# Kernel optimization log

Measured on AMD Instinct MI355X. Metric: run time of the kernel, lower is better.

Reference implementation:

```python
import jax, jax.numpy as jnp
from jax import lax
import numpy as np

B, S, D, H2, V = 1024, 256, 128, 5, 50257
EPS = 1e-5


def setup_inputs() -> dict:
    key = jax.random.key(0)
    ks = jax.random.split(key, 12)
    s = 0.08  # init scale ~ 1/sqrt(D)
    return {
        "x": jax.random.randint(ks[0], (B, S), 0, V),
        "emb": jax.random.normal(ks[1], (V, D), jnp.float32) * s,
        "W_ih1": jax.random.normal(ks[2], (D, D), jnp.float32) * s,
        "b_ih1": jax.random.normal(ks[3], (D,), jnp.float32) * s,
        "W_hh1": jax.random.normal(ks[4], (D, D), jnp.float32) * s,
        "b_hh1": jax.random.normal(ks[5], (D,), jnp.float32) * s,
        "g1": jnp.ones((D,), jnp.float32),
        "be1": jnp.zeros((D,), jnp.float32),
        "W_ih2": jax.random.normal(ks[6], (H2, D), jnp.float32) * s,
        "b_ih2": jax.random.normal(ks[7], (H2,), jnp.float32) * s,
        "W_hh2": jax.random.normal(ks[8], (H2, H2), jnp.float32) * s,
        "b_hh2": jax.random.normal(ks[9], (H2,), jnp.float32) * s,
        "g2": jnp.ones((H2,), jnp.float32),
        "be2": jnp.zeros((H2,), jnp.float32),
    }


def _rnn(xproj, W_hh):
    """Vanilla tanh RNN. xproj: [B,S,H] = x @ W_ih^T + b_ih + b_hh (precomputed)."""
    h0 = jnp.zeros((xproj.shape[0], W_hh.shape[0]), xproj.dtype)

    def step(h, xt):  # xt: [B,H]
        h = jnp.tanh(xt + h @ W_hh.T)
        return h, h

    _, hs = lax.scan(step, h0, jnp.swapaxes(xproj, 0, 1))  # [S,B,H]
    return jnp.swapaxes(hs, 0, 1)  # [B,S,H]


def _ln(z, g, b):
    m = jnp.mean(z, axis=-1, keepdims=True)
    v = jnp.mean(jnp.square(z - m), axis=-1, keepdims=True)
    return (z - m) * lax.rsqrt(v + EPS) * g + b


def reference(x, emb, W_ih1, b_ih1, W_hh1, b_hh1, g1, be1,
              W_ih2, b_ih2, W_hh2, b_hh2, g2, be2):
    e = emb[x]  # [B,S,D]
    z = _rnn(e @ W_ih1.T + (b_ih1 + b_hh1), W_hh1)
    z = _ln(z, g1, be1)
    z = _rnn(z @ W_ih2.T + (b_ih2 + b_hh2), W_hh2)  # [B,S,5]
    z = _ln(z, g2, be2)
    pooled = jnp.mean(z, axis=1)  # AvgPool1d over full seq -> [B,5]
    return jax.nn.softmax(pooled, axis=1)
```

## Files before the change

kernel.cpp:

```cpp
#include <hip/hip_runtime.h>
#include <stdint.h>

#define S_LEN 256
#define DIM   128
#define EPSL  1e-5f

typedef __bf16 bf16x8 __attribute__((ext_vector_type(8)));
typedef float  f32x4  __attribute__((ext_vector_type(4)));

__device__ __forceinline__ unsigned short f2bf_bits(float f) {
  union { float f; unsigned int u; } v; v.f = f;
  unsigned int r = v.u + 0x7fffu + ((v.u >> 16) & 1u);
  return (unsigned short)(r >> 16);
}
__device__ __forceinline__ unsigned f2bf_rhu(float f) {
  return (__float_as_uint(f) + 0x8000u) >> 16;
}
__device__ __forceinline__ unsigned pack_rhu(float lo, float hi) {
  return __builtin_amdgcn_perm(__float_as_uint(hi) + 0x8000u,
                               __float_as_uint(lo) + 0x8000u, 0x07060302u);
}
__device__ __forceinline__ float tanh_fast(float x) {
  float e = __expf(2.f * x);
  return 1.f - 2.f * __builtin_amdgcn_rcpf(e + 1.f);
}

template<int CTRL>
__device__ __forceinline__ float dpp_rot_add(float v) {
  int r = __builtin_amdgcn_update_dpp(0, __float_as_int(v), CTRL, 0xF, 0xF, true);
  return v + __int_as_float(r);
}
template<int CTRL>
__device__ __forceinline__ float dpp_rot_max(float v) {
  int r = __builtin_amdgcn_update_dpp(0, __float_as_int(v), CTRL, 0xF, 0xF, true);
  return fmaxf(v, __int_as_float(r));
}
__device__ __forceinline__ float dpp_sum16(float v) {
  v = dpp_rot_add<0x124>(v); v = dpp_rot_add<0x128>(v);
  v = dpp_rot_add<0x39>(v);  v = dpp_rot_add<0x4E>(v);
  return v;
}
__device__ __forceinline__ float dpp_max16(float v) {
  v = dpp_rot_max<0x124>(v); v = dpp_rot_max<0x128>(v);
  v = dpp_rot_max<0x39>(v);  v = dpp_rot_max<0x4E>(v);
  return v;
}
template<int CTRL>
__device__ __forceinline__ void red_level7(float& s, float& sq, float* d) {
  s  = dpp_rot_add<CTRL>(s);
  sq = dpp_rot_add<CTRL>(sq);
#pragma unroll
  for (int j = 0; j < 5; j++) d[j] = dpp_rot_add<CTRL>(d[j]);
}
template<int JJ>
__device__ __forceinline__ float bcast16(float v) {
  int r = __builtin_amdgcn_ds_swizzle(__float_as_int(v), (JJ << 5) | 0x10);
  return __int_as_float(r);
}

union Frag8 { unsigned short us[8]; bf16x8 v; int4 i4; };

__global__ __launch_bounds__(512, 2)
void rnn_main(const int* __restrict__ x, const float* __restrict__ emb,
              const float* __restrict__ Wih1, const float* __restrict__ bih1,
              const float* __restrict__ Whh1, const float* __restrict__ bhh1,
              const float* __restrict__ g1, const float* __restrict__ be1,
              const float* __restrict__ Wih2, const float* __restrict__ bih2,
              const float* __restrict__ Whh2, const float* __restrict__ bhh2,
              const float* __restrict__ g2, const float* __restrict__ be2,
              unsigned short* __restrict__ hout, int* flags,
              float* __restrict__ out)
{
  __shared__ __align__(16) unsigned short h_bf[2][16 * 128];
  __shared__ __align__(16) unsigned short e_bf[2][16 * 128];
  __shared__ int x_tile[16 * 256];
  __shared__ __align__(16) float p_lds[8][2][32][8];

  const int tid  = threadIdx.x;
  const int wave = tid >> 6;
  const int lane = tid & 63;
  const int l15  = lane & 15;
  const int q    = lane >> 4;

  if (blockIdx.x < 64) {
    const int r0 = blockIdx.x * 16;
    for (int i = tid; i < 16 * 256; i += 512)
      x_tile[i] = x[(size_t)(r0 + (i >> 8)) * S_LEN + (i & 255)];
    for (int i = tid; i < 16 * 128; i += 512) h_bf[1][i] = 0;

    const int n1 = wave * 16 + l15;
    const float bias1v = bih1[n1] + bhh1[n1];
    bf16x8 wh[4], wih[4];
#pragma unroll
    for (int kt = 0; kt < 4; kt++) {
      int k0 = kt * 32 + q * 8;
      Frag8 fh, fa;
#pragma unroll
      for (int j = 0; j < 8; j++) {
        fh.us[j] = f2bf_bits(Whh1[n1 * DIM + k0 + j]);
        fa.us[j] = f2bf_bits(Wih1[n1 * DIM + k0 + j]);
      }
      wh[kt] = fh.v; wih[kt] = fa.v;
    }

    const int srow = wave * 2 + (lane >> 5);
    const int soct = (lane >> 1) & 15;
    const int ssub = lane & 1;
    const int sdst = srow * 128 + ((soct ^ srow) & 15) * 8 + ssub * 4;
    float4 pf[2];
    __syncthreads();

    {
      float4 ta, tb;
      { int xid = x_tile[srow * 256 + 0];
        ta = *(const float4*)(emb + (size_t)xid * DIM + soct * 8 + ssub * 4); }
      { int xid = x_tile[srow * 256 + 1];
        tb = *(const float4*)(emb + (size_t)xid * DIM + soct * 8 + ssub * 4); }
      { int xid = x_tile[srow * 256 + 2];
        pf[0] = *(const float4*)(emb + (size_t)xid * DIM + soct * 8 + ssub * 4); }
      { int xid = x_tile[srow * 256 + 3];
        pf[1] = *(const float4*)(emb + (size_t)xid * DIM + soct * 8 + ssub * 4); }
      int2 pa, pb;
      pa.x = (int)pack_rhu(ta.x, ta.y); pa.y = (int)pack_rhu(ta.z, ta.w);
      pb.x = (int)pack_rhu(tb.x, tb.y); pb.y = (int)pack_rhu(tb.z, tb.w);
      *(int2*)&e_bf[0][sdst] = pa;
      *(int2*)&e_bf[1][sdst] = pb;
    }
    __syncthreads();

    f32x4 xpacc = {bias1v, bias1v, bias1v, bias1v};
#pragma unroll
    for (int kt = 0; kt < 4; kt++) {
      int sw = (((kt * 4 + q) ^ l15) & 15) * 8;
      bf16x8 ae = *(const bf16x8*)&e_bf[0][l15 * 128 + sw];
      xpacc = __builtin_amdgcn_mfma_f32_16x16x32_bf16(ae, wih[kt], xpacc, 0, 0, 0);
    }
    asm volatile("s_waitcnt lgkmcnt(0)\n\ts_barrier" ::: "memory");

#pragma unroll 2
    for (int t = 0; t < S_LEN; t++) {
      f32x4 acc = xpacc;
      {
        const int rb = (t + 1) & 1;
#pragma unroll
        for (int kt = 0; kt < 4; kt++) {
          int sw = (((kt * 4 + q) ^ l15) & 15) * 8;
          bf16x8 ahf = *(const bf16x8*)&h_bf[rb][l15 * 128 + sw];
          acc = __builtin_amdgcn_mfma_f32_16x16x32_bf16(ahf, wh[kt], acc, 0, 0, 0);
        }
        const int wb = t & 1;
        const int oct = n1 >> 3;
#pragma unroll
        for (int r = 0; r < 4; r++) {
          int row = q * 4 + r;
          unsigned short us = (unsigned short)f2bf_rhu(tanh_fast(acc[r]));
          h_bf[wb][row * 128 + ((oct ^ row) & 15) * 8 + (n1 & 7)] = us;
          hout[((size_t)(r0 + row) * S_LEN + t) * DIM + n1] = us;
        }
      }

      if (t + 1 < S_LEN) {
        f32x4 a = {bias1v, bias1v, bias1v, bias1v};
#pragma unroll
        for (int kt = 0; kt < 4; kt++) {
          int sw = (((kt * 4 + q) ^ l15) & 15) * 8;
          bf16x8 ae = *(const bf16x8*)&e_bf[(t + 1) & 1][l15 * 128 + sw];
          a = __builtin_amdgcn_mfma_f32_16x16x32_bf16(ae, wih[kt], a, 0, 0, 0);
        }
        xpacc = a;
      }

      {
        if (t + 2 < S_LEN) {
          int2 pk;
          pk.x = (int)pack_rhu(pf[t & 1].x, pf[t & 1].y);
          pk.y = (int)pack_rhu(pf[t & 1].z, pf[t & 1].w);
          *(int2*)&e_bf[t & 1][sdst] = pk;
        }
        if (t + 4 < S_LEN) {
          int xid = x_tile[srow * 256 + t + 4];
          pf[t & 1] = *(const float4*)(emb + (size_t)xid * DIM + soct * 8 + ssub * 4);
        }
      }
      if (flags != nullptr && (t & 31) == 31)
        asm volatile("s_waitcnt vmcnt(0)" ::: "memory");
      asm volatile("s_waitcnt lgkmcnt(0)\n\ts_barrier" ::: "memory");
      if (flags != nullptr && (t & 31) == 31 && tid == 0)
        __hip_atomic_store(&flags[blockIdx.x * 8 + (t >> 5)], (t >> 5) + 1,
                           __ATOMIC_RELEASE, __HIP_MEMORY_SCOPE_AGENT);
    }
  } else {
    const int bt = blockIdx.x - 64;
    float w2g[5][8], Gs[5], Bs[5], wrow[5];
#pragma unroll
    for (int j = 0; j < 8; j++) {
      int c = l15 * 8 + j;
      float gc = g1[c];
#pragma unroll
      for (int jj = 0; jj < 5; jj++) w2g[jj][j] = Wih2[jj * DIM + c] * gc;
    }
#pragma unroll
    for (int jj = 0; jj < 5; jj++) { Gs[jj] = 0.f; Bs[jj] = 0.f; }
    for (int c = 0; c < DIM; c++) {
      float gc = g1[c], bc = be1[c];
#pragma unroll
      for (int jj = 0; jj < 5; jj++) {
        float w = Wih2[jj * DIM + c];
        Gs[jj] += w * gc; Bs[jj] += w * bc;
      }
    }
    const float validf = (l15 < 5) ? 1.f : 0.f;
    float t2_l = 0.f, g2_l = 0.f, be2_l = 0.f;
    if (l15 < 5) {
      t2_l = bih2[l15] + bhh2[l15];
      g2_l = g2[l15]; be2_l = be2[l15];
#pragma unroll
      for (int jj = 0; jj < 5; jj++) wrow[jj] = Whh2[l15 * 5 + jj];
    } else {
#pragma unroll
      for (int jj = 0; jj < 5; jj++) wrow[jj] = 0.f;
    }
    float h2rep[5] = {0, 0, 0, 0, 0}, pool_l = 0.f;
    const int row_l = 2 * wave + (q & 1);
    const unsigned short* hb =
        hout + (size_t)(bt * 16 + row_l) * S_LEN * DIM;
    const int idx = (l15 < 5) ? l15 : 0;

    for (int c8 = 0; c8 < 8; c8++) {
      if (tid == 0) {
        while (__hip_atomic_load(&flags[bt * 8 + c8], __ATOMIC_RELAXED,
                                 __HIP_MEMORY_SCOPE_AGENT) < c8 + 1)
          __builtin_amdgcn_s_sleep(2);
      }
      __syncthreads();
      __builtin_amdgcn_fence(__ATOMIC_ACQUIRE, "agent");
      for (int tt = 0; tt < 16; tt++) {
        int toff = tt * 2 + (q >> 1);
        uint4 cur = *(const uint4*)(hb + (size_t)(c8 * 32 + toff) * DIM + l15 * 8);
        float hv[8];
        hv[0] = __uint_as_float(cur.x << 16); hv[1] = __uint_as_float(cur.x & 0xffff0000u);
        hv[2] = __uint_as_float(cur.y << 16); hv[3] = __uint_as_float(cur.y & 0xffff0000u);
        hv[4] = __uint_as_float(cur.z << 16); hv[5] = __uint_as_float(cur.z & 0xffff0000u);
        hv[6] = __uint_as_float(cur.w << 16); hv[7] = __uint_as_float(cur.w & 0xffff0000u);
        float s = 0.f, sq = 0.f, d[5] = {0, 0, 0, 0, 0};
#pragma unroll
        for (int j = 0; j < 8; j++) {
          float v = hv[j];
          s += v; sq += v * v;
#pragma unroll
          for (int jj = 0; jj < 5; jj++) d[jj] = fmaf(w2g[jj][j], v, d[jj]);
        }
        red_level7<0x124>(s, sq, d);
        red_level7<0x128>(s, sq, d);
        red_level7<0x39>(s, sq, d);
        red_level7<0x4E>(s, sq, d);
        float mean = s * (1.f / 128.f);
        float var  = sq * (1.f / 128.f) - mean * mean;
        float rstd = rsqrtf(var + EPSL);
        float p[5];
#pragma unroll
        for (int jj = 0; jj < 5; jj++)
          p[jj] = rstd * (d[jj] - mean * Gs[jj]) + Bs[jj];
        float psel = (l15 == 0) ? p[0] : (l15 == 1) ? p[1] :
                     (l15 == 2) ? p[2] : (l15 == 3) ? p[3] : p[4];
        if (l15 < 5) p_lds[wave][q & 1][toff][l15] = psel;
      }
      asm volatile("s_waitcnt lgkmcnt(0)" ::: "memory");
      for (int s = 0; s < 32; s++) {
        float pv = p_lds[wave][q & 1][s][idx];
        float a = pv + t2_l;
#pragma unroll
        for (int jj = 0; jj < 5; jj++) a = fmaf(wrow[jj], h2rep[jj], a);
        float xn = tanh_fast(a);
        float s2 = dpp_sum16(xn * validf) * 0.2f;
        float dd = xn - s2;
        float v2 = dpp_sum16(dd * dd * validf) * 0.2f;
        float r2 = rsqrtf(v2 + EPSL);
        pool_l += dd * r2 * g2_l + be2_l;
        h2rep[0] = bcast16<0>(xn); h2rep[1] = bcast16<1>(xn);
        h2rep[2] = bcast16<2>(xn); h2rep[3] = bcast16<3>(xn);
        h2rep[4] = bcast16<4>(xn);
      }
    }
    float lg = pool_l * (1.f / 256.f);
    float mx = dpp_max16((l15 < 5) ? lg : -3.0e38f);
    float e  = (l15 < 5) ? __expf(lg - mx) : 0.f;
    float sm = dpp_sum16(e);
    if (q < 2 && l15 < 5)
      out[(size_t)(bt * 16 + row_l) * 5 + l15] = e / sm;
  }
}

__global__ __launch_bounds__(256, 2)
void rnn_tail_r11(const unsigned short* __restrict__ hall,
                  const float* __restrict__ g1,  const float* __restrict__ be1,
                  const float* __restrict__ Wih2, const float* __restrict__ bih2,
                  const float* __restrict__ Whh2, const float* __restrict__ bhh2,
                  const float* __restrict__ g2,  const float* __restrict__ be2,
                  float* __restrict__ out)
{
  __shared__ float p_lds[4][4][8];
  const int tid  = threadIdx.x;
  const int wave = tid >> 6;
  const int lane = tid & 63;
  const int l15  = lane & 15;
  const int q    = lane >> 4;
  const int b    = blockIdx.x * 4 + wave;

  float w2g[5][8], Gs[5], Bs[5], wrow[5];
#pragma unroll
  for (int j = 0; j < 8; j++) {
    int c = l15 * 8 + j;
    float gc = g1[c];
#pragma unroll
    for (int jj = 0; jj < 5; jj++) w2g[jj][j] = Wih2[jj * DIM + c] * gc;
  }
#pragma unroll
  for (int jj = 0; jj < 5; jj++) { Gs[jj] = 0.f; Bs[jj] = 0.f; }
  for (int c = 0; c < DIM; c++) {
    float gc = g1[c], bc = be1[c];
#pragma unroll
    for (int jj = 0; jj < 5; jj++) {
      float w = Wih2[jj * DIM + c];
      Gs[jj] += w * gc; Bs[jj] += w * bc;
    }
  }
  const float validf = (l15 < 5) ? 1.f : 0.f;
  float t2_l = 0.f, g2_l = 0.f, be2_l = 0.f;
  if (l15 < 5) {
    t2_l = bih2[l15] + bhh2[l15];
    g2_l = g2[l15]; be2_l = be2[l15];
#pragma unroll
    for (int jj = 0; jj < 5; jj++) wrow[jj] = Whh2[l15 * 5 + jj];
  } else {
#pragma unroll
    for (int jj = 0; jj < 5; jj++) wrow[jj] = 0.f;
  }
  float h2rep[5];
#pragma unroll
  for (int jj = 0; jj < 5; jj++) h2rep[jj] = 0.f;
  float pool_l = 0.f;

  const unsigned short* hb = hall + (size_t)b * S_LEN * DIM;
  uint4 hpre = *(const uint4*)(hb + (size_t)q * DIM + l15 * 8);

  for (int t0 = 0; t0 < S_LEN; t0 += 4) {
    uint4 cur = hpre;
    if (t0 + 4 < S_LEN)
      hpre = *(const uint4*)(hb + (size_t)(t0 + 4 + q) * DIM + l15 * 8);
    float hv[8];
    hv[0] = __uint_as_float(cur.x << 16); hv[1] = __uint_as_float(cur.x & 0xffff0000u);
    hv[2] = __uint_as_float(cur.y << 16); hv[3] = __uint_as_float(cur.y & 0xffff0000u);
    hv[4] = __uint_as_float(cur.z << 16); hv[5] = __uint_as_float(cur.z & 0xffff0000u);
    hv[6] = __uint_as_float(cur.w << 16); hv[7] = __uint_as_float(cur.w & 0xffff0000u);
    float s = 0.f, sq = 0.f, d[5] = {0, 0, 0, 0, 0};
#pragma unroll
    for (int j = 0; j < 8; j++) {
      float v = hv[j];
      s += v; sq += v * v;
#pragma unroll
      for (int jj = 0; jj < 5; jj++) d[jj] = fmaf(w2g[jj][j], v, d[jj]);
    }
    red_level7<0x124>(s, sq, d);
    red_level7<0x128>(s, sq, d);
    red_level7<0x39>(s, sq, d);
    red_level7<0x4E>(s, sq, d);
    float mean = s * (1.f / 128.f);
    float var  = sq * (1.f / 128.f) - mean * mean;
    float rstd = rsqrtf(var + EPSL);
    float p[5];
#pragma unroll
    for (int jj = 0; jj < 5; jj++)
      p[jj] = rstd * (d[jj] - mean * Gs[jj]) + Bs[jj];
    float psel = (l15 == 0) ? p[0] : (l15 == 1) ? p[1] :
                 (l15 == 2) ? p[2] : (l15 == 3) ? p[3] : p[4];
    if (l15 < 5) p_lds[wave][q][l15] = psel;
    asm volatile("s_waitcnt lgkmcnt(0)" ::: "memory");
    const int idx = (l15 < 5) ? l15 : 0;
#pragma unroll
    for (int g = 0; g < 4; g++) {
      float pv = p_lds[wave][g][idx];
      float a = pv + t2_l;
#pragma unroll
      for (int jj = 0; jj < 5; jj++) a = fmaf(wrow[jj], h2rep[jj], a);
      float xn = tanh_fast(a);
      float s2 = dpp_sum16(xn * validf) * 0.2f;
      float dd = xn - s2;
      float v2 = dpp_sum16(dd * dd * validf) * 0.2f;
      float r2 = rsqrtf(v2 + EPSL);
      pool_l += dd * r2 * g2_l + be2_l;
      h2rep[0] = bcast16<0>(xn); h2rep[1] = bcast16<1>(xn);
      h2rep[2] = bcast16<2>(xn); h2rep[3] = bcast16<3>(xn);
      h2rep[4] = bcast16<4>(xn);
    }
  }

  float lg = pool_l * (1.f / 256.f);
  float mx = dpp_max16((l15 < 5) ? lg : -3.0e38f);
  float e  = (l15 < 5) ? __expf(lg - mx) : 0.f;
  float sm = dpp_sum16(e);
  if (q == 0 && l15 < 5) out[(size_t)b * 5 + l15] = e / sm;
}

extern "C" void kernel_launch(void* const* d_in, const int* in_sizes, int n_in,
                              void* d_out, int out_size, void* d_ws, size_t ws_size,
                              hipStream_t stream) {
  (void)in_sizes; (void)n_in; (void)out_size;
  const int*   x    = (const int*)  d_in[0];
  const float* emb  = (const float*)d_in[1];
  const float* Wih1 = (const float*)d_in[2];
  const float* bih1 = (const float*)d_in[3];
  const float* Whh1 = (const float*)d_in[4];
  const float* bhh1 = (const float*)d_in[5];
  const float* g1   = (const float*)d_in[6];
  const float* be1  = (const float*)d_in[7];
  const float* Wih2 = (const float*)d_in[8];
  const float* bih2 = (const float*)d_in[9];
  const float* Whh2 = (const float*)d_in[10];
  const float* bhh2 = (const float*)d_in[11];
  const float* g2   = (const float*)d_in[12];
  const float* be2  = (const float*)d_in[13];
  float* out = (float*)d_out;

  const size_t HBYTES = (size_t)1024 * S_LEN * DIM * 2;
  unsigned short* hws = (unsigned short*)d_ws;

  if (ws_size >= HBYTES + 4096) {
    int* flags = (int*)((char*)d_ws + HBYTES);
    rnn_main<<<dim3(128), dim3(512), 0, stream>>>(
        x, emb, Wih1, bih1, Whh1, bhh1, g1, be1,
        Wih2, bih2, Whh2, bhh2, g2, be2, hws, flags, out);
  } else {
    rnn_main<<<dim3(64), dim3(512), 0, stream>>>(
        x, emb, Wih1, bih1, Whh1, bhh1, g1, be1,
        Wih2, bih2, Whh2, bhh2, g2, be2, hws, nullptr, out);
    rnn_tail_r11<<<dim3(256), dim3(256), 0, stream>>>(
        hws, g1, be1, Wih2, bih2, Whh2, bhh2, g2, be2, out);
  }
}
```

Measured before the change: 256.1 us.

## Run each layer-1 RNN recurrence in a single wave without block barriers

The layer-1 recurrence moves from a 512-thread block of 16 rows, where 8 waves each own 16 output columns and sync via s_barrier every step, to a single wave per block that owns all 128 columns for 8 rows (half the MFMA rows padded). Weights for all 8 column tiles are held in registers, embeddings are loaded straight into MFMA fragments with a two-step software pipeline, and hidden-state stores to global are issued from LDS reads. The aim is to remove the per-step block barrier and spread the recurrence over twice as many CUs, at the cost of heavy register pressure, wasted MFMA rows, and fewer threads per CU. The consumer blocks are remapped to 8 rows per block.

After: 523.5 us. 104% more time.

```diff
diff --git a/kernel.cpp b/kernel.cpp
--- a/kernel.cpp
+++ b/kernel.cpp
@@ -60,137 +60,173 @@
 
 union Frag8 { unsigned short us[8]; bf16x8 v; int4 i4; };
 
-__global__ __launch_bounds__(512, 2)
-void rnn_main(const int* __restrict__ x, const float* __restrict__ emb,
-              const float* __restrict__ Wih1, const float* __restrict__ bih1,
-              const float* __restrict__ Whh1, const float* __restrict__ bhh1,
-              const float* __restrict__ g1, const float* __restrict__ be1,
-              const float* __restrict__ Wih2, const float* __restrict__ bih2,
-              const float* __restrict__ Whh2, const float* __restrict__ bhh2,
-              const float* __restrict__ g2, const float* __restrict__ be2,
-              unsigned short* __restrict__ hout, int* flags,
-              float* __restrict__ out)
+__global__ __launch_bounds__(256, 1)
+void rnn_wavecore(const int* __restrict__ x, const float* __restrict__ emb,
+                  const float* __restrict__ Wih1, const float* __restrict__ bih1,
+                  const float* __restrict__ Whh1, const float* __restrict__ bhh1,
+                  const float* __restrict__ g1, const float* __restrict__ be1,
+                  const float* __restrict__ Wih2, const float* __restrict__ bih2,
+                  const float* __restrict__ Whh2, const float* __restrict__ bhh2,
+                  const float* __restrict__ g2, const float* __restrict__ be2,
+                  unsigned short* __restrict__ hout, int* flags,
+                  float* __restrict__ out)
 {
-  __shared__ __align__(16) unsigned short h_bf[2][16 * 128];
-  __shared__ __align__(16) unsigned short e_bf[2][16 * 128];
-  __shared__ int x_tile[16 * 256];
-  __shared__ __align__(16) float p_lds[8][2][32][8];
+  __shared__ __align__(16) unsigned short h_priv[16 * 128];
+  __shared__ __align__(16) float p_lds[4][2][32][8];
 
   const int tid  = threadIdx.x;
-  const int wave = tid >> 6;
   const int lane = tid & 63;
   const int l15  = lane & 15;
   const int q    = lane >> 4;
 
-  if (blockIdx.x < 64) {
-    const int r0 = blockIdx.x * 16;
-    for (int i = tid; i < 16 * 256; i += 512)
-      x_tile[i] = x[(size_t)(r0 + (i >> 8)) * S_LEN + (i & 255)];
-    for (int i = tid; i < 16 * 128; i += 512) h_bf[1][i] = 0;
-
-    const int n1 = wave * 16 + l15;
-    const float bias1v = bih1[n1] + bhh1[n1];
-    bf16x8 wh[4], wih[4];
-#pragma unroll
-    for (int kt = 0; kt < 4; kt++) {
-      int k0 = kt * 32 + q * 8;
-      Frag8 fh, fa;
-#pragma unroll
-      for (int j = 0; j < 8; j++) {
-        fh.us[j] = f2bf_bits(Whh1[n1 * DIM + k0 + j]);
-        fa.us[j] = f2bf_bits(Wih1[n1 * DIM + k0 + j]);
-      }
-      wh[kt] = fh.v; wih[kt] = fa.v;
-    }
-
-    const int srow = wave * 2 + (lane >> 5);
-    const int soct = (lane >> 1) & 15;
-    const int ssub = lane & 1;
-    const int sdst = srow * 128 + ((soct ^ srow) & 15) * 8 + ssub * 4;
-    float4 pf[2];
-    __syncthreads();
+  if (blockIdx.x < 128) {
+    if (tid >= 64) return;
+    const int r0   = blockIdx.x * 8;
+    const bool arow = ((l15 & 2) == 0);
+    const int rowi  = ((l15 >> 2) << 1) | (l15 & 1);
+    const size_t growu = (size_t)(r0 + rowi);
 
     {
-      float4 ta, tb;
-      { int xid = x_tile[srow * 256 + 0];
-        ta = *(const float4*)(emb + (size_t)xid * DIM + soct * 8 + ssub * 4); }
-      { int xid = x_tile[srow * 256 + 1];
-        tb = *(const float4*)(emb + (size_t)xid * DIM + soct * 8 + ssub * 4); }
-      { int xid = x_tile[srow * 256 + 2];
-        pf[0] = *(const float4*)(emb + (size_t)xid * DIM + soct * 8 + ssub * 4); }
-      { int xid = x_tile[srow * 256 + 3];
-        pf[1] = *(const float4*)(emb + (size_t)xid * DIM + soct * 8 + ssub * 4); }
-      int2 pa, pb;
-      pa.x = (int)pack_rhu(ta.x, ta.y); pa.y = (int)pack_rhu(ta.z, ta.w);
-      pb.x = (int)pack_rhu(tb.x, tb.y); pb.y = (int)pack_rhu(tb.z, tb.w);
-      *(int2*)&e_bf[0][sdst] = pa;
-      *(int2*)&e_bf[1][sdst] = pb;
-    }
-    __syncthreads();
-
-    f32x4 xpacc = {bias1v, bias1v, bias1v, bias1v};
-#pragma unroll
-    for (int kt = 0; kt < 4; kt++) {
-      int sw = (((kt * 4 + q) ^ l15) & 15) * 8;
-      bf16x8 ae = *(const bf16x8*)&e_bf[0][l15 * 128 + sw];
-      xpacc = __builtin_amdgcn_mfma_f32_16x16x32_bf16(ae, wih[kt], xpacc, 0, 0, 0);
-    }
-    asm volatile("s_waitcnt lgkmcnt(0)\n\ts_barrier" ::: "memory");
-
-#pragma unroll 2
-    for (int t = 0; t < S_LEN; t++) {
-      f32x4 acc = xpacc;
-      {
-        const int rb = (t + 1) & 1;
-#pragma unroll
-        for (int kt = 0; kt < 4; kt++) {
-          int sw = (((kt * 4 + q) ^ l15) & 15) * 8;
-          bf16x8 ahf = *(const bf16x8*)&h_bf[rb][l15 * 128 + sw];
-          acc = __builtin_amdgcn_mfma_f32_16x16x32_bf16(ahf, wh[kt], acc, 0, 0, 0);
+      int4 z = {0, 0, 0, 0};
+#pragma unroll
+      for (int i = 0; i < 4; i++)
+        *(int4*)&h_priv[(i * 64 + lane) * 8] = z;
+    }
+
+    float biasx[8];
+    bf16x8 whh[8][4], wih[8][4];
+#pragma unroll
+    for (int tile = 0; tile < 8; tile++) {
+      const int d = tile * 16 + l15;
+      biasx[tile] = bih1[d] + bhh1[d];
+#pragma unroll
+      for (int kt = 0; kt < 4; kt++) {
+        Frag8 fh, fa;
+#pragma unroll
+        for (int j = 0; j < 8; j++) {
+          fh.us[j] = f2bf_bits(Whh1[d * DIM + kt * 32 + q * 8 + j]);
+          fa.us[j] = f2bf_bits(Wih1[d * DIM + kt * 32 + q * 8 + j]);
         }
-        const int wb = t & 1;
-        const int oct = n1 >> 3;
-#pragma unroll
-        for (int r = 0; r < 4; r++) {
-          int row = q * 4 + r;
-          unsigned short us = (unsigned short)f2bf_rhu(tanh_fast(acc[r]));
-          h_bf[wb][row * 128 + ((oct ^ row) & 15) * 8 + (n1 & 7)] = us;
-          hout[((size_t)(r0 + row) * S_LEN + t) * DIM + n1] = us;
+        whh[tile][kt] = fh.v; wih[tile][kt] = fa.v;
+      }
+    }
+
+    int ra[4];
+#pragma unroll
+    for (int kt = 0; kt < 4; kt++)
+      ra[kt] = l15 * 128 + (((kt * 4 + q) ^ l15) & 15) * 8;
+
+    auto eload = [&](float4* eld, int xid) {
+      const float* pe = emb + (size_t)xid * DIM + q * 8;
+#pragma unroll
+      for (int kt = 0; kt < 4; kt++) {
+        eld[kt * 2]     = *(const float4*)(pe + kt * 32);
+        eld[kt * 2 + 1] = *(const float4*)(pe + kt * 32 + 4);
+      }
+    };
+    auto epack = [&](Frag8* frag, const float4* eld) {
+#pragma unroll
+      for (int kt = 0; kt < 4; kt++) {
+        frag[kt].i4.x = (int)pack_rhu(eld[kt * 2].x,     eld[kt * 2].y);
+        frag[kt].i4.y = (int)pack_rhu(eld[kt * 2].z,     eld[kt * 2].w);
+        frag[kt].i4.z = (int)pack_rhu(eld[kt * 2 + 1].x, eld[kt * 2 + 1].y);
+        frag[kt].i4.w = (int)pack_rhu(eld[kt * 2 + 1].z, eld[kt * 2 + 1].w);
+      }
+    };
+    auto produce = [&](f32x4* xp, const Frag8* frag) {
+#pragma unroll
+      for (int tile = 0; tile < 8; tile++) {
+        f32x4 a = {biasx[tile], biasx[tile], biasx[tile], biasx[tile]};
+#pragma unroll
+        for (int kt = 0; kt < 4; kt++)
+          a = __builtin_amdgcn_mfma_f32_16x16x32_bf16(frag[kt].v, wih[tile][kt], a, 0, 0, 0);
+        xp[tile] = a;
+      }
+    };
+    auto sstep = [&](int t, const f32x4* xp) {
+      bf16x8 ha[4];
+#pragma unroll
+      for (int kt = 0; kt < 4; kt++)
+        ha[kt] = *(const bf16x8*)&h_priv[ra[kt]];
+      if (t > 0 && arow) {
+        unsigned short* hp = hout + (growu * S_LEN + (t - 1)) * DIM + q * 8;
+#pragma unroll
+        for (int kt = 0; kt < 4; kt++)
+          *(int4*)(hp + kt * 32) = *(const int4*)&ha[kt];
+      }
+#pragma unroll
+      for (int tile = 0; tile < 8; tile++) {
+        f32x4 acc = xp[tile];
+#pragma unroll
+        for (int kt = 0; kt < 4; kt++)
+          acc = __builtin_amdgcn_mfma_f32_16x16x32_bf16(ha[kt], whh[tile][kt], acc, 0, 0, 0);
+        const int oct = tile * 2 + (l15 >> 3);
+#pragma unroll
+        for (int r = 0; r < 2; r++) {
+          const int m = q * 4 + r;
+          h_priv[m * 128 + ((oct ^ m) & 15) * 8 + (l15 & 7)] =
+              (unsigned short)f2bf_rhu(tanh_fast(acc[r]));
         }
       }
-
-      if (t + 1 < S_LEN) {
-        f32x4 a = {bias1v, bias1v, bias1v, bias1v};
-#pragma unroll
-        for (int kt = 0; kt < 4; kt++) {
-          int sw = (((kt * 4 + q) ^ l15) & 15) * 8;
-          bf16x8 ae = *(const bf16x8*)&e_bf[(t + 1) & 1][l15 * 128 + sw];
-          a = __builtin_amdgcn_mfma_f32_16x16x32_bf16(ae, wih[kt], a, 0, 0, 0);
-        }
-        xpacc = a;
-      }
-
-      {
-        if (t + 2 < S_LEN) {
-          int2 pk;
-          pk.x = (int)pack_rhu(pf[t & 1].x, pf[t & 1].y);
-          pk.y = (int)pack_rhu(pf[t & 1].z, pf[t & 1].w);
-          *(int2*)&e_bf[t & 1][sdst] = pk;
-        }
-        if (t + 4 < S_LEN) {
-          int xid = x_tile[srow * 256 + t + 4];
-          pf[t & 1] = *(const float4*)(emb + (size_t)xid * DIM + soct * 8 + ssub * 4);
-        }
-      }
-      if (flags != nullptr && (t & 31) == 31)
+    };
+
+    float4 eldA[8], eldB[8];
+    Frag8  frag[4];
+    f32x4  xpA[8], xpB[8];
+    int xidA, xidB;
+    {
+      int xid0 = x[growu * S_LEN + 0];
+      eload(eldA, xid0); epack(frag, eldA); produce(xpA, frag);
+      int xid1 = x[growu * S_LEN + 1];
+      eload(eldA, xid1); epack(frag, eldA);
+      int xid2 = x[growu * S_LEN + 2];
+      eload(eldA, xid2);
+      int xid3 = x[growu * S_LEN + 3];
+      eload(eldB, xid3);
+      xidA = x[growu * S_LEN + 4];
+      xidB = x[growu * S_LEN + 5];
+    }
+
+    for (int tp = 0; tp < S_LEN / 2; tp++) {
+      const int t0 = 2 * tp, t1 = t0 + 1;
+      sstep(t0, xpA);
+      if (flags != nullptr && t0 > 0 && (t0 & 31) == 0) {
         asm volatile("s_waitcnt vmcnt(0)" ::: "memory");
-      asm volatile("s_waitcnt lgkmcnt(0)\n\ts_barrier" ::: "memory");
-      if (flags != nullptr && (t & 31) == 31 && tid == 0)
-        __hip_atomic_store(&flags[blockIdx.x * 8 + (t >> 5)], (t >> 5) + 1,
-                           __ATOMIC_RELEASE, __HIP_MEMORY_SCOPE_AGENT);
+        if (lane == 0)
+          __hip_atomic_store(&flags[blockIdx.x * 8 + (t0 >> 5) - 1], t0 >> 5,
+                             __ATOMIC_RELEASE, __HIP_MEMORY_SCOPE_AGENT);
+      }
+      if (t0 + 1 < S_LEN) produce(xpB, frag);
+      if (t0 + 2 < S_LEN) epack(frag, eldA);
+      if (t0 + 4 < S_LEN) eload(eldA, xidA);
+      if (t0 + 6 < S_LEN) xidA = x[growu * S_LEN + t0 + 6];
+      sstep(t1, xpB);
+      if (t1 + 1 < S_LEN) produce(xpA, frag);
+      if (t1 + 2 < S_LEN) epack(frag, eldB);
+      if (t1 + 4 < S_LEN) eload(eldB, xidB);
+      if (t1 + 6 < S_LEN) xidB = x[growu * S_LEN + t1 + 6];
+    }
+    {
+      bf16x8 ha[4];
+#pragma unroll
+      for (int kt = 0; kt < 4; kt++)
+        ha[kt] = *(const bf16x8*)&h_priv[ra[kt]];
+      if (arow) {
+        unsigned short* hp = hout + (growu * S_LEN + (S_LEN - 1)) * DIM + q * 8;
+#pragma unroll
+        for (int kt = 0; kt < 4; kt++)
+          *(int4*)(hp + kt * 32) = *(const int4*)&ha[kt];
+      }
+      if (flags != nullptr) {
+        asm volatile("s_waitcnt vmcnt(0)" ::: "memory");
+        if (lane == 0)
+          __hip_atomic_store(&flags[blockIdx.x * 8 + 7], 8,
+                             __ATOMIC_RELEASE, __HIP_MEMORY_SCOPE_AGENT);
+      }
     }
   } else {
-    const int bt = blockIdx.x - 64;
+    const int bt = blockIdx.x - 128;
+    const int wave = tid >> 6;
     float w2g[5][8], Gs[5], Bs[5], wrow[5];
 #pragma unroll
     for (int j = 0; j < 8; j++) {
@@ -221,9 +257,8 @@
       for (int jj = 0; jj < 5; jj++) wrow[jj] = 0.f;
     }
     float h2rep[5] = {0, 0, 0, 0, 0}, pool_l = 0.f;
-    const int row_l = 2 * wave + (q & 1);
-    const unsigned short* hb =
-        hout + (size_t)(bt * 16 + row_l) * S_LEN * DIM;
+    const int rowg = bt * 8 + wave * 2 + (q & 1);
+    const unsigned short* hb = hout + (size_t)rowg * S_LEN * DIM;
     const int idx = (l15 < 5) ? l15 : 0;
 
     for (int c8 = 0; c8 < 8; c8++) {
@@ -287,7 +322,7 @@
     float e  = (l15 < 5) ? __expf(lg - mx) : 0.f;
     float sm = dpp_sum16(e);
     if (q < 2 && l15 < 5)
-      out[(size_t)(bt * 16 + row_l) * 5 + l15] = e / sm;
+      out[(size_t)rowg * 5 + l15] = e / sm;
   }
 }
 
@@ -427,11 +462,11 @@
 
   if (ws_size >= HBYTES + 4096) {
     int* flags = (int*)((char*)d_ws + HBYTES);
-    rnn_main<<<dim3(128), dim3(512), 0, stream>>>(
+    rnn_wavecore<<<dim3(256), dim3(256), 0, stream>>>(
         x, emb, Wih1, bih1, Whh1, bhh1, g1, be1,
         Wih2, bih2, Whh2, bhh2, g2, be2, hws, flags, out);
   } else {
-    rnn_main<<<dim3(64), dim3(512), 0, stream>>>(
+    rnn_wavecore<<<dim3(128), dim3(256), 0, stream>>>(
         x, emb, Wih1, bih1, Whh1, bhh1, g1, be1,
         Wih2, bih2, Whh2, bhh2, g2, be2, hws, nullptr, out);
     rnn_tail_r11<<<dim3(256), dim3(256), 0, stream>>>(
```

## Precompute layer-1 input projection into global buffer before recurrence loop

Applied to the files above, without the earlier changes.

Adds a new kernel where each producer block first computes the full embedding-gather plus W_ih1 projection for all 256 timesteps with MFMA and writes the results to a global workspace buffer. The recurrent loop then only reads one precomputed fragment per step, so embedding loads and input-projection MFMAs leave the serial critical path. The consumer blocks run the LN plus second RNN from flag-synchronised hidden states as before. This needs about 128MB of extra workspace and adds a large global write and read-back, and it is used only when the workspace is large enough.

Measured after the change: 355.2 us. +38.7%, slower.

```diff
diff --git a/kernel.cpp b/kernel.cpp
--- a/kernel.cpp
+++ b/kernel.cpp
@@ -59,6 +59,241 @@
 }
 
 union Frag8 { unsigned short us[8]; bf16x8 v; int4 i4; };
+
+__global__ __launch_bounds__(512, 2)
+void rnn_xp(const int* __restrict__ x, const float* __restrict__ emb,
+            const float* __restrict__ Wih1, const float* __restrict__ bih1,
+            const float* __restrict__ Whh1, const float* __restrict__ bhh1,
+            const float* __restrict__ g1, const float* __restrict__ be1,
+            const float* __restrict__ Wih2, const float* __restrict__ bih2,
+            const float* __restrict__ Whh2, const float* __restrict__ bhh2,
+            const float* __restrict__ g2, const float* __restrict__ be2,
+            unsigned short* __restrict__ hout, int* flags,
+            float* __restrict__ xpg, float* __restrict__ out)
+{
+  __shared__ __align__(16) unsigned short h_bf[2][16 * 128];
+  __shared__ int x_tile[16 * 256];
+  __shared__ __align__(16) float p_lds[8][2][32][8];
+
+  const int tid  = threadIdx.x;
+  const int wave = tid >> 6;
+  const int lane = tid & 63;
+  const int l15  = lane & 15;
+  const int q    = lane >> 4;
+
+  if (blockIdx.x < 64) {
+    const int r0 = blockIdx.x * 16;
+    float* xpb = xpg + (size_t)blockIdx.x * (S_LEN * 8 * 64 * 4);
+
+    for (int i = tid; i < 16 * 256; i += 512)
+      x_tile[i] = x[(size_t)(r0 + (i >> 8)) * S_LEN + (i & 255)];
+    __syncthreads();
+
+    {
+      float biasx[8];
+      bf16x8 wihA[8][4];
+#pragma unroll
+      for (int tile = 0; tile < 8; tile++) {
+        const int d = tile * 16 + l15;
+        biasx[tile] = bih1[d] + bhh1[d];
+#pragma unroll
+        for (int kt = 0; kt < 4; kt++) {
+          Frag8 fa;
+#pragma unroll
+          for (int j = 0; j < 8; j++)
+            fa.us[j] = f2bf_bits(Wih1[d * DIM + kt * 32 + q * 8 + j]);
+          wihA[tile][kt] = fa.v;
+        }
+      }
+      const int t0w = wave * 32;
+      float4 eldA[8], eldB[8];
+      auto eload = [&](float4* e, int t) {
+        int xid = x_tile[l15 * 256 + t];
+        const float* pe = emb + (size_t)xid * DIM + q * 8;
+#pragma unroll
+        for (int kt = 0; kt < 4; kt++) {
+          e[kt * 2]     = *(const float4*)(pe + kt * 32);
+          e[kt * 2 + 1] = *(const float4*)(pe + kt * 32 + 4);
+        }
+      };
+      auto p1step = [&](int s, float4* ecur) {
+        Frag8 fr[4];
+#pragma unroll
+        for (int kt = 0; kt < 4; kt++) {
+          fr[kt].i4.x = (int)pack_rhu(ecur[kt * 2].x,     ecur[kt * 2].y);
+          fr[kt].i4.y = (int)pack_rhu(ecur[kt * 2].z,     ecur[kt * 2].w);
+          fr[kt].i4.z = (int)pack_rhu(ecur[kt * 2 + 1].x, ecur[kt * 2 + 1].y);
+          fr[kt].i4.w = (int)pack_rhu(ecur[kt * 2 + 1].z, ecur[kt * 2 + 1].w);
+        }
+        if (s + 2 < 32) eload(ecur, t0w + s + 2);
+#pragma unroll
+        for (int tile = 0; tile < 8; tile++) {
+          f32x4 a = {biasx[tile], biasx[tile], biasx[tile], biasx[tile]};
+#pragma unroll
+          for (int kt = 0; kt < 4; kt++)
+            a = __builtin_amdgcn_mfma_f32_16x16x32_bf16(fr[kt].v, wihA[tile][kt], a, 0, 0, 0);
+          *(f32x4*)(xpb + (((size_t)(t0w + s) * 8 + tile) * 64 + lane) * 4) = a;
+        }
+      };
+      eload(eldA, t0w); eload(eldB, t0w + 1);
+      for (int s = 0; s < 32; s += 2) {
+        p1step(s, eldA);
+        p1step(s + 1, eldB);
+      }
+    }
+    asm volatile("s_waitcnt vmcnt(0)" ::: "memory");
+    __syncthreads();
+
+    for (int i = tid; i < 16 * 128; i += 512) h_bf[1][i] = 0;
+    const int n1 = wave * 16 + l15;
+    bf16x8 wh[4];
+#pragma unroll
+    for (int kt = 0; kt < 4; kt++) {
+      Frag8 fh;
+#pragma unroll
+      for (int j = 0; j < 8; j++)
+        fh.us[j] = f2bf_bits(Whh1[n1 * DIM + kt * 32 + q * 8 + j]);
+      wh[kt] = fh.v;
+    }
+    const float* xpw = xpb + ((size_t)wave * 64 + lane) * 4;
+    f32x4 xprA = *(const f32x4*)(xpw + (size_t)0 * 2048);
+    f32x4 xprB = *(const f32x4*)(xpw + (size_t)1 * 2048);
+    asm volatile("s_waitcnt lgkmcnt(0)\n\ts_barrier" ::: "memory");
+
+    auto sstep = [&](int t, const f32x4 xpcur) {
+      f32x4 acc = xpcur;
+      const int rb = (t + 1) & 1;
+#pragma unroll
+      for (int kt = 0; kt < 4; kt++) {
+        int sw = (((kt * 4 + q) ^ l15) & 15) * 8;
+        bf16x8 ahf = *(const bf16x8*)&h_bf[rb][l15 * 128 + sw];
+        acc = __builtin_amdgcn_mfma_f32_16x16x32_bf16(ahf, wh[kt], acc, 0, 0, 0);
+      }
+      const int wb = t & 1;
+      const int oct = n1 >> 3;
+#pragma unroll
+      for (int r = 0; r < 4; r++) {
+        int row = q * 4 + r;
+        unsigned short us = (unsigned short)f2bf_rhu(tanh_fast(acc[r]));
+        h_bf[wb][row * 128 + ((oct ^ row) & 15) * 8 + (n1 & 7)] = us;
+        hout[((size_t)(r0 + row) * S_LEN + t) * DIM + n1] = us;
+      }
+      if (flags != nullptr && (t & 31) == 31)
+        asm volatile("s_waitcnt vmcnt(0)" ::: "memory");
+      asm volatile("s_waitcnt lgkmcnt(0)\n\ts_barrier" ::: "memory");
+      if (flags != nullptr && (t & 31) == 31 && tid == 0)
+        __hip_atomic_store(&flags[blockIdx.x * 8 + (t >> 5)], (t >> 5) + 1,
+                           __ATOMIC_RELEASE, __HIP_MEMORY_SCOPE_AGENT);
+    };
+
+    for (int tp = 0; tp < S_LEN / 2; tp++) {
+      const int t0 = 2 * tp, t1 = t0 + 1;
+      sstep(t0, xprA);
+      if (t0 + 2 < S_LEN) xprA = *(const f32x4*)(xpw + (size_t)(t0 + 2) * 2048);
+      sstep(t1, xprB);
+      if (t1 + 2 < S_LEN) xprB = *(const f32x4*)(xpw + (size_t)(t1 + 2) * 2048);
+    }
+  } else {
+    const int bt = blockIdx.x - 64;
+    float w2g[5][8], Gs[5], Bs[5], wrow[5];
+#pragma unroll
+    for (int j = 0; j < 8; j++) {
+      int c = l15 * 8 + j;
+      float gc = g1[c];
+#pragma unroll
+      for (int jj = 0; jj < 5; jj++) w2g[jj][j] = Wih2[jj * DIM + c] * gc;
+    }
+#pragma unroll
+    for (int jj = 0; jj < 5; jj++) { Gs[jj] = 0.f; Bs[jj] = 0.f; }
+    for (int c = 0; c < DIM; c++) {
+      float gc = g1[c], bc = be1[c];
+#pragma unroll
+      for (int jj = 0; jj < 5; jj++) {
+        float w = Wih2[jj * DIM + c];
+        Gs[jj] += w * gc; Bs[jj] += w * bc;
+      }
+    }
+    const float validf = (l15 < 5) ? 1.f : 0.f;
+    float t2_l = 0.f, g2_l = 0.f, be2_l = 0.f;
+    if (l15 < 5) {
+      t2_l = bih2[l15] + bhh2[l15];
+      g2_l = g2[l15]; be2_l = be2[l15];
+#pragma unroll
+      for (int jj = 0; jj < 5; jj++) wrow[jj] = Whh2[l15 * 5 + jj];
+    } else {
+#pragma unroll
+      for (int jj = 0; jj < 5; jj++) wrow[jj] = 0.f;
+    }
+    float h2rep[5] = {0, 0, 0, 0, 0}, pool_l = 0.f;
+    const int row_l = 2 * wave + (q & 1);
+    const unsigned short* hb =
+        hout + (size_t)(bt * 16 + row_l) * S_LEN * DIM;
+    const int idx = (l15 < 5) ? l15 : 0;
+
+    for (int c8 = 0; c8 < 8; c8++) {
+      if (tid == 0) {
+        while (__hip_atomic_load(&flags[bt * 8 + c8], __ATOMIC_RELAXED,
+                                 __HIP_MEMORY_SCOPE_AGENT) < c8 + 1)
+          __builtin_amdgcn_s_sleep(2);
+      }
+      __syncthreads();
+      __builtin_amdgcn_fence(__ATOMIC_ACQUIRE, "agent");
+      for (int tt = 0; tt < 16; tt++) {
+        int toff = tt * 2 + (q >> 1);
+        uint4 cur = *(const uint4*)(hb + (size_t)(c8 * 32 + toff) * DIM + l15 * 8);
+        float hv[8];
+        hv[0] = __uint_as_float(cur.x << 16); hv[1] = __uint_as_float(cur.x & 0xffff0000u);
+        hv[2] = __uint_as_float(cur.y << 16); hv[3] = __uint_as_float(cur.y & 0xffff0000u);
+        hv[4] = __uint_as_float(cur.z << 16); hv[5] = __uint_as_float(cur.z & 0xffff0000u);
+        hv[6] = __uint_as_float(cur.w << 16); hv[7] = __uint_as_float(cur.w & 0xffff0000u);
+        float s = 0.f, sq = 0.f, d[5] = {0, 0, 0, 0, 0};
+#pragma unroll
+        for (int j = 0; j < 8; j++) {
+          float v = hv[j];
+          s += v; sq += v * v;
+#pragma unroll
+          for (int jj = 0; jj < 5; jj++) d[jj] = fmaf(w2g[jj][j], v, d[jj]);
+        }
+        red_level7<0x124>(s, sq, d);
+        red_level7<0x128>(s, sq, d);
+        red_level7<0x39>(s, sq, d);
+        red_level7<0x4E>(s, sq, d);
+        float mean = s * (1.f / 128.f);
+        float var  = sq * (1.f / 128.f) - mean * mean;
+        float rstd = rsqrtf(var + EPSL);
+        float p[5];
+#pragma unroll
+        for (int jj = 0; jj < 5; jj++)
+          p[jj] = rstd * (d[jj] - mean * Gs[jj]) + Bs[jj];
+        float psel = (l15 == 0) ? p[0] : (l15 == 1) ? p[1] :
+                     (l15 == 2) ? p[2] : (l15 == 3) ? p[3] : p[4];
+        if (l15 < 5) p_lds[wave][q & 1][toff][l15] = psel;
+      }
+      asm volatile("s_waitcnt lgkmcnt(0)" ::: "memory");
+      for (int s = 0; s < 32; s++) {
+        float pv = p_lds[wave][q & 1][s][idx];
+        float a = pv + t2_l;
+#pragma unroll
+        for (int jj = 0; jj < 5; jj++) a = fmaf(wrow[jj], h2rep[jj], a);
+        float xn = tanh_fast(a);
+        float s2 = dpp_sum16(xn * validf) * 0.2f;
+        float dd = xn - s2;
+        float v2 = dpp_sum16(dd * dd * validf) * 0.2f;
+        float r2 = rsqrtf(v2 + EPSL);
+        pool_l += dd * r2 * g2_l + be2_l;
+        h2rep[0] = bcast16<0>(xn); h2rep[1] = bcast16<1>(xn);
+        h2rep[2] = bcast16<2>(xn); h2rep[3] = bcast16<3>(xn);
+        h2rep[4] = bcast16<4>(xn);
+      }
+    }
+    float lg = pool_l * (1.f / 256.f);
+    float mx = dpp_max16((l15 < 5) ? lg : -3.0e38f);
+    float e  = (l15 < 5) ? __expf(lg - mx) : 0.f;
+    float sm = dpp_sum16(e);
+    if (q < 2 && l15 < 5)
+      out[(size_t)(bt * 16 + row_l) * 5 + l15] = e / sm;
+  }
+}
 
 __global__ __launch_bounds__(512, 2)
 void rnn_main(const int* __restrict__ x, const float* __restrict__ emb,
@@ -422,10 +657,17 @@
   const float* be2  = (const float*)d_in[13];
   float* out = (float*)d_out;
 
-  const size_t HBYTES = (size_t)1024 * S_LEN * DIM * 2;
+  const size_t HBYTES  = (size_t)1024 * S_LEN * DIM * 2;
+  const size_t XPBYTES = (size_t)64 * S_LEN * 8 * 64 * 16;
   unsigned short* hws = (unsigned short*)d_ws;
 
-  if (ws_size >= HBYTES + 4096) {
+  if (ws_size >= HBYTES + 4096 + XPBYTES) {
+    int*   flags = (int*)((char*)d_ws + HBYTES);
+    float* xpg   = (float*)((char*)d_ws + HBYTES + 4096);
+    rnn_xp<<<dim3(128), dim3(512), 0, stream>>>(
+        x, emb, Wih1, bih1, Whh1, bhh1, g1, be1,
+        Wih2, bih2, Whh2, bhh2, g2, be2, hws, flags, xpg, out);
+  } else if (ws_size >= HBYTES + 4096) {
     int* flags = (int*)((char*)d_ws + HBYTES);
     rnn_main<<<dim3(128), dim3(512), 0, stream>>>(
         x, emb, Wih1, bih1, Whh1, bhh1, g1, be1,
```

## Load embedding rows directly into MFMA fragments, removing LDS staging buffer

Applied to the files above, without the earlier changes.

Each lane now gathers its own embedding slice straight from global memory into registers, packs it to bf16 MFMA A-fragments, and computes the input projection without the shared e_bf staging buffer. Loads run four steps ahead using two register sets (A/B), and the time loop is manually unrolled by two. This removes LDS writes and reads of embeddings from the serial recurrence critical path and shrinks the LDS footprint. In exchange, every wave redundantly loads the same 16 embedding rows, which raises global/L2 traffic and register pressure.

Result: slower. 585.5 us (+128.6%).

```diff
diff --git a/kernel.cpp b/kernel.cpp
--- a/kernel.cpp
+++ b/kernel.cpp
@@ -72,7 +72,6 @@
               float* __restrict__ out)
 {
   __shared__ __align__(16) unsigned short h_bf[2][16 * 128];
-  __shared__ __align__(16) unsigned short e_bf[2][16 * 128];
   __shared__ int x_tile[16 * 256];
   __shared__ __align__(16) float p_lds[8][2][32][8];
 
@@ -102,91 +101,81 @@
       }
       wh[kt] = fh.v; wih[kt] = fa.v;
     }
-
-    const int srow = wave * 2 + (lane >> 5);
-    const int soct = (lane >> 1) & 15;
-    const int ssub = lane & 1;
-    const int sdst = srow * 128 + ((soct ^ srow) & 15) * 8 + ssub * 4;
-    float4 pf[2];
     __syncthreads();
 
-    {
-      float4 ta, tb;
-      { int xid = x_tile[srow * 256 + 0];
-        ta = *(const float4*)(emb + (size_t)xid * DIM + soct * 8 + ssub * 4); }
-      { int xid = x_tile[srow * 256 + 1];
-        tb = *(const float4*)(emb + (size_t)xid * DIM + soct * 8 + ssub * 4); }
-      { int xid = x_tile[srow * 256 + 2];
-        pf[0] = *(const float4*)(emb + (size_t)xid * DIM + soct * 8 + ssub * 4); }
-      { int xid = x_tile[srow * 256 + 3];
-        pf[1] = *(const float4*)(emb + (size_t)xid * DIM + soct * 8 + ssub * 4); }
-      int2 pa, pb;
-      pa.x = (int)pack_rhu(ta.x, ta.y); pa.y = (int)pack_rhu(ta.z, ta.w);
-      pb.x = (int)pack_rhu(tb.x, tb.y); pb.y = (int)pack_rhu(tb.z, tb.w);
-      *(int2*)&e_bf[0][sdst] = pa;
-      *(int2*)&e_bf[1][sdst] = pb;
-    }
-    __syncthreads();
-
-    f32x4 xpacc = {bias1v, bias1v, bias1v, bias1v};
-#pragma unroll
-    for (int kt = 0; kt < 4; kt++) {
-      int sw = (((kt * 4 + q) ^ l15) & 15) * 8;
-      bf16x8 ae = *(const bf16x8*)&e_bf[0][l15 * 128 + sw];
-      xpacc = __builtin_amdgcn_mfma_f32_16x16x32_bf16(ae, wih[kt], xpacc, 0, 0, 0);
-    }
+    float4 eldA[8], eldB[8];
+    Frag8  frag[4];
+    auto eload = [&](float4* e, int xid) {
+      const float* pe = emb + (size_t)xid * DIM + q * 8;
+#pragma unroll
+      for (int kt = 0; kt < 4; kt++) {
+        e[kt * 2]     = *(const float4*)(pe + kt * 32);
+        e[kt * 2 + 1] = *(const float4*)(pe + kt * 32 + 4);
+      }
+    };
+    auto epack = [&](const float4* e) {
+#pragma unroll
+      for (int kt = 0; kt < 4; kt++) {
+        frag[kt].i4.x = (int)pack_rhu(e[kt * 2].x,     e[kt * 2].y);
+        frag[kt].i4.y = (int)pack_rhu(e[kt * 2].z,     e[kt * 2].w);
+        frag[kt].i4.z = (int)pack_rhu(e[kt * 2 + 1].x, e[kt * 2 + 1].y);
+        frag[kt].i4.w = (int)pack_rhu(e[kt * 2 + 1].z, e[kt * 2 + 1].w);
+      }
+    };
+    f32x4 xpacc;
+    auto produce = [&]() {
+      f32x4 a = {bias1v, bias1v, bias1v, bias1v};
+#pragma unroll
+      for (int kt = 0; kt < 4; kt++)
+        a = __builtin_amdgcn_mfma_f32_16x16x32_bf16(frag[kt].v, wih[kt], a, 0, 0, 0);
+      xpacc = a;
+    };
+    auto sstep = [&](int t) {
+      f32x4 acc = xpacc;
+      const int rb = (t + 1) & 1;
+#pragma unroll
+      for (int kt = 0; kt < 4; kt++) {
+        int sw = (((kt * 4 + q) ^ l15) & 15) * 8;
+        bf16x8 ahf = *(const bf16x8*)&h_bf[rb][l15 * 128 + sw];
+        acc = __builtin_amdgcn_mfma_f32_16x16x32_bf16(ahf, wh[kt], acc, 0, 0, 0);
+      }
+      const int wb = t & 1;
+      const int oct = n1 >> 3;
+#pragma unroll
+      for (int r = 0; r < 4; r++) {
+        int row = q * 4 + r;
+        unsigned short us = (unsigned short)f2bf_rhu(tanh_fast(acc[r]));
+        h_bf[wb][row * 128 + ((oct ^ row) & 15) * 8 + (n1 & 7)] = us;
+        hout[((size_t)(r0 + row) * S_LEN + t) * DIM + n1] = us;
+      }
+    };
+
+    eload(eldA, x_tile[l15 * 256 + 0]); epack(eldA); produce();
+    eload(eldA, x_tile[l15 * 256 + 1]); epack(eldA);
+    eload(eldA, x_tile[l15 * 256 + 2]);
+    eload(eldB, x_tile[l15 * 256 + 3]);
+    int xidA = x_tile[l15 * 256 + 4];
+    int xidB = x_tile[l15 * 256 + 5];
     asm volatile("s_waitcnt lgkmcnt(0)\n\ts_barrier" ::: "memory");
 
-#pragma unroll 2
-    for (int t = 0; t < S_LEN; t++) {
-      f32x4 acc = xpacc;
-      {
-        const int rb = (t + 1) & 1;
-#pragma unroll
-        for (int kt = 0; kt < 4; kt++) {
-          int sw = (((kt * 4 + q) ^ l15) & 15) * 8;
-          bf16x8 ahf = *(const bf16x8*)&h_bf[rb][l15 * 128 + sw];
-          acc = __builtin_amdgcn_mfma_f32_16x16x32_bf16(ahf, wh[kt], acc, 0, 0, 0);
-        }
-        const int wb = t & 1;
-        const int oct = n1 >> 3;
-#pragma unroll
-        for (int r = 0; r < 4; r++) {
-          int row = q * 4 + r;
-          unsigned short us = (unsigned short)f2bf_rhu(tanh_fast(acc[r]));
-          h_bf[wb][row * 128 + ((oct ^ row) & 15) * 8 + (n1 & 7)] = us;
-          hout[((size_t)(r0 + row) * S_LEN + t) * DIM + n1] = us;
-        }
-      }
-
-      if (t + 1 < S_LEN) {
-        f32x4 a = {bias1v, bias1v, bias1v, bias1v};
-#pragma unroll
-        for (int kt = 0; kt < 4; kt++) {
-          int sw = (((kt * 4 + q) ^ l15) & 15) * 8;
-          bf16x8 ae = *(const bf16x8*)&e_bf[(t + 1) & 1][l15 * 128 + sw];
-          a = __builtin_amdgcn_mfma_f32_16x16x32_bf16(ae, wih[kt], a, 0, 0, 0);
-        }
-        xpacc = a;
-      }
-
-      {
-        if (t + 2 < S_LEN) {
-          int2 pk;
-          pk.x = (int)pack_rhu(pf[t & 1].x, pf[t & 1].y);
-          pk.y = (int)pack_rhu(pf[t & 1].z, pf[t & 1].w);
-          *(int2*)&e_bf[t & 1][sdst] = pk;
-        }
-        if (t + 4 < S_LEN) {
-          int xid = x_tile[srow * 256 + t + 4];
-          pf[t & 1] = *(const float4*)(emb + (size_t)xid * DIM + soct * 8 + ssub * 4);
-        }
-      }
-      if (flags != nullptr && (t & 31) == 31)
+    for (int tp = 0; tp < S_LEN / 2; tp++) {
+      const int t0 = 2 * tp, t1 = t0 + 1;
+      sstep(t0);
+      produce();
+      if (t0 + 2 < S_LEN) epack(eldA);
+      if (t0 + 4 < S_LEN) eload(eldA, xidA);
+      if (t0 + 6 < S_LEN) xidA = x_tile[l15 * 256 + t0 + 6];
+      asm volatile("s_waitcnt lgkmcnt(0)\n\ts_barrier" ::: "memory");
+      sstep(t1);
+      if (t1 + 1 < S_LEN) produce();
+      if (t1 + 2 < S_LEN) epack(eldB);
+      if (t1 + 4 < S_LEN) eload(eldB, xidB);
+      if (t1 + 6 < S_LEN) xidB = x_tile[l15 * 256 + t1 + 6];
+      if (flags != nullptr && (t1 & 31) == 31)
         asm volatile("s_waitcnt vmcnt(0)" ::: "memory");
       asm volatile("s_waitcnt lgkmcnt(0)\n\ts_barrier" ::: "memory");
-      if (flags != nullptr && (t & 31) == 31 && tid == 0)
-        __hip_atomic_store(&flags[blockIdx.x * 8 + (t >> 5)], (t >> 5) + 1,
+      if (flags != nullptr && (t1 & 31) == 31 && tid == 0)
+        __hip_atomic_store(&flags[blockIdx.x * 8 + (t1 >> 5)], (t1 >> 5) + 1,
                            __ATOMIC_RELEASE, __HIP_MEMORY_SCOPE_AGENT);
     }
   } else {
```
